# Optimization experiments

Measured on AMD Instinct MI355X. Metric: run time of the kernel, lower is better.

The kernel has to match this reference:

```python
import jax, jax.numpy as jnp
import numpy as np
import math

B, H, L, DK = 4, 12, 1024, 64
GLOBAL, LOCAL, INIT_VAL = 8, 4, 8
W = INIT_VAL + 1  # window length fed to each GRU
MAX_VAL = 1.0e12


def setup_inputs() -> dict:
    k0 = jax.random.key(0)
    ks = jax.random.split(k0, 9)
    bound = 1.0 / math.sqrt(DK)
    uni = lambda k, shape: jax.random.uniform(k, shape, jnp.float32, -bound, bound)
    return {
        "query": jax.random.normal(ks[0], (B, H, L, DK), jnp.float32),
        "key": jax.random.normal(ks[1], (B, H, L, DK), jnp.float32),
        "value": jax.random.normal(ks[2], (B, H, L, DK), jnp.float32),
        "mask": jax.random.randint(ks[3], (B, 1, L, L), 0, 2, jnp.int32),
        # per-local-head GRU parameters (torch nn.GRU layout: gates [r, z, n])
        "w_ih": uni(ks[4], (LOCAL, 3 * DK, DK)),
        "w_hh": uni(ks[5], (LOCAL, 3 * DK, DK)),
        "b_ih": uni(ks[6], (LOCAL, 3 * DK)),
        "b_hh": uni(ks[7], (LOCAL, 3 * DK)),
    }


def reference(query, key, value, mask, w_ih, w_hh, b_ih, b_hh):
    b, h, l, d_k = query.shape
    # ---- global softmax-attention heads ----
    q_g, k_g, v_g = query[:, :GLOBAL], key[:, :GLOBAL], value[:, :GLOBAL]
    scores = jnp.einsum('bhqd,bhkd->bhqk', q_g, k_g) / math.sqrt(d_k)
    scores = jnp.where(mask == 0, -MAX_VAL, scores)
    p_attn = jax.nn.softmax(scores, axis=-1)
    out_g = jnp.einsum('bhqk,bhkd->bhqd', p_attn, v_g)  # (b, GLOBAL, l, d_k)

    # ---- local heads: windowed value gather ----
    v_l = value[:, GLOBAL:]                                   # (b, LOCAL, l, d_k)
    v_pad = jnp.pad(v_l, ((0, 0), (0, 0), (0, INIT_VAL), (0, 0)))
    dist = jnp.arange(l)[:, None] + jnp.arange(W)[None, :]    # (l, W) forward window
    v_aug = v_pad[:, :, dist, :]                              # (b, LOCAL, l, W, d_k)
    x = v_aug.reshape(b * LOCAL * l, W, d_k)                  # all windows, shared by every GRU

    # ---- per-head GRU over the window; keep last hidden state ----
    def gru_last_hidden(wih, whh, bih, bhh):
        xg = jnp.einsum('ntd,gd->ntg', x, wih) + bih          # (N, W, 3*d_k), input gates precomputed
        def step(hc, xg_t):
            gh = hc @ whh.T + bhh
            xr, xz, xn = jnp.split(xg_t, 3, axis=-1)
            hr, hz, hn = jnp.split(gh, 3, axis=-1)
            r = jax.nn.sigmoid(xr + hr)
            z = jax.nn.sigmoid(xz + hz)
            n_ = jnp.tanh(xn + r * hn)
            return (1.0 - z) * n_ + z * hc, None
        h0 = jnp.zeros((x.shape[0], d_k), x.dtype)
        hT, _ = jax.lax.scan(step, h0, jnp.swapaxes(xg, 0, 1))
        return hT                                             # (N, d_k)

    hs = jax.vmap(gru_last_hidden)(w_ih, w_hh, b_ih, b_hh)    # (LOCAL, N, d_k)
    # faithful to torch cat: GRU i applied to ALL local heads -> LOCAL*LOCAL output heads
    out_l = hs.reshape(LOCAL, b, LOCAL, l, d_k).transpose(1, 0, 2, 3, 4)
    out_l = out_l.reshape(b, LOCAL * LOCAL, l, d_k)

    return jnp.concatenate([out_g, out_l], axis=1)            # (b, GLOBAL + LOCAL^2, l, d_k)
```

## Files before the change

### kernel.cpp

```cpp
#include <hip/hip_runtime.h>

#define B_  4
#define H_  12
#define L_  1024
#define DK_ 64
#define GH_ 8
#define WS_ 9

#define ATTN_LDS_BYTES (3 * 64 * 64 * 2)
#define GRU_W_OFF    0
#define GRU_XGP_OFF  24576
#define GRU_BIH_OFF  77888
#define GRU_BHH_OFF  78656
#define GRU_LDS_BYTES 79424
#define XGP_STRIDE   392

#define MB_WORDS (B_ * L_ * 16)

typedef __attribute__((ext_vector_type(8))) short short8;
typedef __attribute__((ext_vector_type(4))) float f32x4;

#define MFMA_BF16(a, b, c) __builtin_amdgcn_mfma_f32_16x16x32_bf16((a), (b), (c), 0, 0, 0)

__device__ __forceinline__ unsigned short f2bf(float f) {
  unsigned int u = __builtin_bit_cast(unsigned int, f);
  u += 0x7fffu + ((u >> 16) & 1u);
  return (unsigned short)(u >> 16);
}
__device__ __forceinline__ float bf2f(unsigned short s) {
  return __builtin_bit_cast(float, ((unsigned int)s) << 16);
}
__device__ __forceinline__ short8 pack8(const float4 a, const float4 b) {
  short8 r;
  r[0] = (short)f2bf(a.x); r[1] = (short)f2bf(a.y);
  r[2] = (short)f2bf(a.z); r[3] = (short)f2bf(a.w);
  r[4] = (short)f2bf(b.x); r[5] = (short)f2bf(b.y);
  r[6] = (short)f2bf(b.z); r[7] = (short)f2bf(b.w);
  return r;
}
__device__ __forceinline__ uint4 packrow16(const float4 a, const float4 b) {
  uint4 r;
  r.x = (unsigned)f2bf(a.x) | ((unsigned)f2bf(a.y) << 16);
  r.y = (unsigned)f2bf(a.z) | ((unsigned)f2bf(a.w) << 16);
  r.z = (unsigned)f2bf(b.x) | ((unsigned)f2bf(b.y) << 16);
  r.w = (unsigned)f2bf(b.z) | ((unsigned)f2bf(b.w) << 16);
  return r;
}
__device__ __forceinline__ float bfget(const uint2 u, const int r) {
  const unsigned d = (r & 2) ? u.y : u.x;
  return (r & 1) ? __builtin_bit_cast(float, d & 0xffff0000u)
                 : __builtin_bit_cast(float, d << 16);
}
__device__ __forceinline__ int pi_row(const int dt, const int m) {
  return ((dt & 1) << 5) + ((m >> 2) << 3) + ((dt >> 1) << 2) + (m & 3);
}

__global__ __launch_bounds__(256) void maskpack_kernel(
    const int* __restrict__ mask, unsigned long long* __restrict__ mb)
{
  const int idx = blockIdx.x * 256 + threadIdx.x;
  const int* src = mask + (size_t)idx * 64;
  unsigned long long bits = 0ull;
#pragma unroll
  for (int i = 0; i < 16; ++i) {
    const int4 m4 = *(const int4*)(src + i * 4);
    if (m4.x) bits |= 1ull << (i * 4 + 0);
    if (m4.y) bits |= 1ull << (i * 4 + 1);
    if (m4.z) bits |= 1ull << (i * 4 + 2);
    if (m4.w) bits |= 1ull << (i * 4 + 3);
  }
  mb[idx] = bits;
}

__global__ __launch_bounds__(256) void attn_kernel(
    const float* __restrict__ q, const float* __restrict__ k,
    const float* __restrict__ v, const int* __restrict__ mask,
    const unsigned long long* __restrict__ mb, const int use_bits,
    float* __restrict__ out)
{
  extern __shared__ char smc[];
  char* sK  = smc;
  char* sVT = smc + 8192;
  char* sP  = smc + 16384;

  const int tid = threadIdx.x;
  const int q0 = blockIdx.x * 64;
  const int h  = blockIdx.y;
  const int b  = blockIdx.z;

  const int w  = tid >> 6;
  const int ln = tid & 63;
  const int lg = ln >> 4;
  const int c  = ln & 15;

  const size_t hbase = ((size_t)b * H_ + h) * L_ * DK_;
  const float* kp = k + hbase;
  const float* vp = v + hbase;
  const int*   mp = mask + (size_t)b * L_ * L_;
  const unsigned long long* mbp = mb + (size_t)b * L_ * 16;

  short8 qa[2];
  {
    const float* qrow = q + hbase + (size_t)(q0 + w * 16 + c) * DK_ + lg * 8;
#pragma unroll
    for (int kt = 0; kt < 2; ++kt) {
      const float4 f0 = *(const float4*)(qrow + kt * 32);
      const float4 f1 = *(const float4*)(qrow + kt * 32 + 4);
      qa[kt] = pack8(f0, f1);
    }
  }

  char* sPw = sP + w * 2048;

  f32x4 o_[4];
#pragma unroll
  for (int nt = 0; nt < 4; ++nt) { o_[nt][0] = 0.f; o_[nt][1] = 0.f; o_[nt][2] = 0.f; o_[nt][3] = 0.f; }
  float mrun[4], lrun[4];
#pragma unroll
  for (int r = 0; r < 4; ++r) { mrun[r] = -1e30f; lrun[r] = 0.f; }

  const int rr  = tid >> 2;
  const int c16 = (tid & 3) << 4;
  const int r2  = (tid & 31) << 1;
  const int j0v = (tid >> 5) << 3;

  float4 kreg[4], vreg[4];
  unsigned long long mreg[4];
  {
    const float* ksrc = kp + (size_t)rr * DK_ + c16;
    kreg[0] = *(const float4*)(ksrc);      kreg[1] = *(const float4*)(ksrc + 4);
    kreg[2] = *(const float4*)(ksrc + 8);  kreg[3] = *(const float4*)(ksrc + 12);
    const float* vsrc = vp + (size_t)r2 * DK_ + j0v;
    vreg[0] = *(const float4*)(vsrc);       vreg[1] = *(const float4*)(vsrc + 4);
    vreg[2] = *(const float4*)(vsrc + 64);  vreg[3] = *(const float4*)(vsrc + 68);
    if (use_bits) {
#pragma unroll
      for (int r = 0; r < 4; ++r)
        mreg[r] = mbp[(size_t)(q0 + w * 16 + lg * 4 + r) * 16 + 0];
    }
  }

  for (int kt0 = 0; kt0 < 16; ++kt0) {
    {
      const int kb = rr * 128 + c16 * 2;
      const int sw = (rr & 7) << 4;
      *(uint4*)(sK + ((kb) ^ sw))      = packrow16(kreg[0], kreg[1]);
      *(uint4*)(sK + ((kb + 16) ^ sw)) = packrow16(kreg[2], kreg[3]);
      const float va_[8] = {vreg[0].x, vreg[0].y, vreg[0].z, vreg[0].w,
                            vreg[1].x, vreg[1].y, vreg[1].z, vreg[1].w};
      const float vb_[8] = {vreg[2].x, vreg[2].y, vreg[2].z, vreg[2].w,
                            vreg[3].x, vreg[3].y, vreg[3].z, vreg[3].w};
#pragma unroll
      for (int j = 0; j < 8; ++j) {
        const int d = j0v + j;
        const unsigned u32v = (unsigned)f2bf(va_[j]) | ((unsigned)f2bf(vb_[j]) << 16);
        *(unsigned*)(sVT + ((d * 128 + r2 * 2) ^ ((d & 7) << 4))) = u32v;
      }
    }
    asm volatile("s_waitcnt lgkmcnt(0)" ::: "memory");
    __builtin_amdgcn_s_barrier();

    unsigned long long mcur[4];
#pragma unroll
    for (int r = 0; r < 4; ++r) mcur[r] = mreg[r];
    {
      const int ktn = (kt0 + 1) & 15;
      const float* ksrc = kp + (size_t)(ktn * 64 + rr) * DK_ + c16;
      kreg[0] = *(const float4*)(ksrc);      kreg[1] = *(const float4*)(ksrc + 4);
      kreg[2] = *(const float4*)(ksrc + 8);  kreg[3] = *(const float4*)(ksrc + 12);
      const float* vsrc = vp + (size_t)(ktn * 64 + r2) * DK_ + j0v;
      vreg[0] = *(const float4*)(vsrc);       vreg[1] = *(const float4*)(vsrc + 4);
      vreg[2] = *(const float4*)(vsrc + 64);  vreg[3] = *(const float4*)(vsrc + 68);
      if (use_bits) {
#pragma unroll
        for (int r = 0; r < 4; ++r)
          mreg[r] = mbp[(size_t)(q0 + w * 16 + lg * 4 + r) * 16 + ktn];
      }
    }

    f32x4 acc[4];
#pragma unroll
    for (int nt = 0; nt < 4; ++nt) {
      acc[nt][0] = 0.f; acc[nt][1] = 0.f; acc[nt][2] = 0.f; acc[nt][3] = 0.f;
#pragma unroll
      for (int kt = 0; kt < 2; ++kt) {
        const int off = (((nt * 16 + c) * 128 + kt * 64 + lg * 16) ^ ((c & 7) << 4));
        const short8 bk = __builtin_bit_cast(short8, *(const uint4*)(sK + off));
        acc[nt] = MFMA_BF16(qa[kt], bk, acc[nt]);
      }
    }

#pragma unroll
    for (int r = 0; r < 4; ++r) {
      bool k0_, k1_, k2_, k3_;
      if (use_bits) {
        const unsigned long long mword = mcur[r];
        k0_ = (mword >> (c)) & 1ull;
        k1_ = (mword >> (16 + c)) & 1ull;
        k2_ = (mword >> (32 + c)) & 1ull;
        k3_ = (mword >> (48 + c)) & 1ull;
      } else {
        const int qr = q0 + w * 16 + lg * 4 + r;
        const int* mrow = mp + (size_t)qr * L_ + kt0 * 64 + c;
        k0_ = mrow[0] != 0; k1_ = mrow[16] != 0; k2_ = mrow[32] != 0; k3_ = mrow[48] != 0;
      }
      const float s0_ = k0_ ? acc[0][r] * 0.125f : -1e12f;
      const float s1_ = k1_ ? acc[1][r] * 0.125f : -1e12f;
      const float s2_ = k2_ ? acc[2][r] * 0.125f : -1e12f;
      const float s3_ = k3_ ? acc[3][r] * 0.125f : -1e12f;
      float mt = fmaxf(fmaxf(s0_, s1_), fmaxf(s2_, s3_));
#pragma unroll
      for (int off = 1; off < 16; off <<= 1) mt = fmaxf(mt, __shfl_xor(mt, off));
      const float mnew = fmaxf(mrun[r], mt);
      const float p0 = __expf(s0_ - mnew);
      const float p1 = __expf(s1_ - mnew);
      const float p2 = __expf(s2_ - mnew);
      const float p3 = __expf(s3_ - mnew);
      float pt = p0 + p1 + p2 + p3;
#pragma unroll
      for (int off = 1; off < 16; off <<= 1) pt += __shfl_xor(pt, off);
      const float scale = __expf(mrun[r] - mnew);
      mrun[r] = mnew;
      lrun[r] = lrun[r] * scale + pt;
      o_[0][r] *= scale; o_[1][r] *= scale; o_[2][r] *= scale; o_[3][r] *= scale;
      const int prow = lg * 4 + r;
      const int pb = prow * 128;
      const int psw = (prow & 7) << 4;
      *(unsigned short*)(sPw + ((pb + (c * 2)) ^ psw))       = f2bf(p0);
      *(unsigned short*)(sPw + ((pb + (16 + c) * 2) ^ psw))  = f2bf(p1);
      *(unsigned short*)(sPw + ((pb + (32 + c) * 2) ^ psw))  = f2bf(p2);
      *(unsigned short*)(sPw + ((pb + (48 + c) * 2) ^ psw))  = f2bf(p3);
    }

#pragma unroll
    for (int kt = 0; kt < 2; ++kt) {
      const int aoff = ((c * 128 + kt * 64 + lg * 16) ^ ((c & 7) << 4));
      const short8 pa = __builtin_bit_cast(short8, *(const uint4*)(sPw + aoff));
#pragma unroll
      for (int nt = 0; nt < 4; ++nt) {
        const int boff = (((nt * 16 + c) * 128 + kt * 64 + lg * 16) ^ ((c & 7) << 4));
        const short8 bv = __builtin_bit_cast(short8, *(const uint4*)(sVT + boff));
        o_[nt] = MFMA_BF16(pa, bv, o_[nt]);
      }
    }
    asm volatile("s_waitcnt lgkmcnt(0)" ::: "memory");
    __builtin_amdgcn_s_barrier();
  }

  float* op = out + (((size_t)b * 24 + h) * L_ + q0 + w * 16) * DK_;
#pragma unroll
  for (int r = 0; r < 4; ++r) {
    const float inv = 1.f / lrun[r];
#pragma unroll
    for (int nt = 0; nt < 4; ++nt)
      op[(size_t)(lg * 4 + r) * DK_ + nt * 16 + c] = o_[nt][r] * inv;
  }
}

__global__ __launch_bounds__(512, 4) void gru_kernel(
    const float* __restrict__ value, const float* __restrict__ wih_g,
    const float* __restrict__ whh_g, const float* __restrict__ bih_g,
    const float* __restrict__ bhh_g, float* __restrict__ out)
{
  extern __shared__ char smc[];
  char*  sW   = smc + GRU_W_OFF;
  char*  sXGP = smc + GRU_XGP_OFF;
  float* sBih = (float*)(smc + GRU_BIH_OFF);
  float* sBhh = (float*)(smc + GRU_BHH_OFF);

  const int tid  = threadIdx.x;
  const int l0   = blockIdx.x * 128;
  const int gset = blockIdx.y >> 2;
  const int vh   = blockIdx.y & 3;
  const int b    = blockIdx.z;

  const float* vp   = value + (((size_t)b * H_ + GH_ + vh) * L_) * DK_;
  const float* wih  = wih_g + (size_t)gset * 192 * DK_;
  const float* whh  = whh_g + (size_t)gset * 192 * DK_;
  const float* bihp = bih_g + gset * 192;
  const float* bhhp = bhh_g + gset * 192;

  if (tid < 192) { sBih[tid] = bihp[tid]; sBhh[tid] = bhhp[tid]; }

  for (int cid = tid; cid < 1536; cid += 512) {
    const int row = cid >> 3, ch = cid & 7;
    const int g = row >> 6, dt = (row >> 4) & 3, m = row & 15;
    const int arow = g * 64 + pi_row(dt, m);
    const float* wp = whh + (size_t)arow * 64 + ch * 8;
    const float4 w0 = *(const float4*)wp;
    const float4 w1 = *(const float4*)(wp + 4);
    *(uint4*)(sW + ((row * 128 + ch * 16) ^ ((row & 7) << 4))) = packrow16(w0, w1);
  }
  __syncthreads();

  const int w  = tid >> 6;
  const int ln = tid & 63;
  const int lg = ln >> 4;
  const int c  = ln & 15;

  for (int t = w; t < 108; t += 8) {
    const int jt = t % 12, pt = t / 12;
    const int g = jt >> 2, dt = jt & 3;
    const int aj = g * 64 + pi_row(dt, c);
    const float* wb = wih + (size_t)aj * 64 + lg * 8;
    const short8 aA = pack8(*(const float4*)(wb),      *(const float4*)(wb + 4));
    const short8 aB = pack8(*(const float4*)(wb + 32), *(const float4*)(wb + 36));
    const int pos = pt * 16 + c;
    const int gp  = l0 + pos;
    const bool valid = gp < L_;
    float4 z4; z4.x = 0.f; z4.y = 0.f; z4.z = 0.f; z4.w = 0.f;
    const float* va = vp + (size_t)gp * 64 + lg * 8;
    const short8 bA = pack8(valid ? *(const float4*)(va)      : z4,
                            valid ? *(const float4*)(va + 4)  : z4);
    const short8 bB = pack8(valid ? *(const float4*)(va + 32) : z4,
                            valid ? *(const float4*)(va + 36) : z4);
    f32x4 acc = {0.f, 0.f, 0.f, 0.f};
    acc = MFMA_BF16(aA, bA, acc);
    acc = MFMA_BF16(aB, bB, acc);
    const int jb = g * 64 + ((dt & 1) << 5) + (lg << 3) + ((dt >> 1) << 2);
    const f32x4 bi = *(const f32x4*)(sBih + jb);
    const f32x4 bh4 = *(const f32x4*)(sBhh + jb);
    const float foldh = (g < 2) ? 1.f : 0.f;
    if (pos < 136) {
      uint2 pk;
      pk.x = (unsigned)f2bf(acc[0] + bi[0] + foldh * bh4[0]) |
             ((unsigned)f2bf(acc[1] + bi[1] + foldh * bh4[1]) << 16);
      pk.y = (unsigned)f2bf(acc[2] + bi[2] + foldh * bh4[2]) |
             ((unsigned)f2bf(acc[3] + bi[3] + foldh * bh4[3]) << 16);
      *(uint2*)(sXGP + pos * XGP_STRIDE + jt * 32 + lg * 8) = pk;
    }
  }
  __syncthreads();

  const int seqB = w * 16;
  const int xrow0 = seqB + c;

  f32x4 bhn[4];
#pragma unroll
  for (int dt = 0; dt < 4; ++dt)
    bhn[dt] = *(const f32x4*)(sBhh + 128 + ((dt & 1) << 5) + (lg << 3) + ((dt >> 1) << 2));

  float hfr[4][4];
  short8 bh[2], bl[2];
#pragma unroll
  for (int dt = 0; dt < 4; ++dt)
#pragma unroll
    for (int r = 0; r < 4; ++r) hfr[dt][r] = 0.f;
#pragma unroll
  for (int kt = 0; kt < 2; ++kt) {
#pragma unroll
    for (int i = 0; i < 8; ++i) { bh[kt][i] = 0; bl[kt][i] = 0; }
  }

  const int swz = (c & 7) << 4;

  for (int ts = 0; ts < WS_; ++ts) {
    const int xbase = (xrow0 + ts) * XGP_STRIDE + lg * 8;

#pragma unroll
    for (int dt = 0; dt < 4; ++dt) {
      const uint2 xgr = *(const uint2*)(sXGP + xbase + dt * 32);
      const uint2 xgz = *(const uint2*)(sXGP + xbase + (4 + dt) * 32);
      const uint2 xgn = *(const uint2*)(sXGP + xbase + (8 + dt) * 32);

      f32x4 ar = {0.f, 0.f, 0.f, 0.f};
      f32x4 az = {0.f, 0.f, 0.f, 0.f};
      f32x4 an = {0.f, 0.f, 0.f, 0.f};
#pragma unroll
      for (int kt = 0; kt < 2; ++kt) {
        const int base = kt * 64 + lg * 16;
        const short8 wr = __builtin_bit_cast(short8,
            *(const uint4*)(sW + ((((dt)     * 16 + c) * 128 + base) ^ swz)));
        const short8 wz = __builtin_bit_cast(short8,
            *(const uint4*)(sW + ((((4 + dt) * 16 + c) * 128 + base) ^ swz)));
        const short8 wn = __builtin_bit_cast(short8,
            *(const uint4*)(sW + ((((8 + dt) * 16 + c) * 128 + base) ^ swz)));
        ar = MFMA_BF16(wr, bh[kt], ar); ar = MFMA_BF16(wr, bl[kt], ar);
        az = MFMA_BF16(wz, bh[kt], az); az = MFMA_BF16(wz, bl[kt], az);
        an = MFMA_BF16(wn, bh[kt], an); an = MFMA_BF16(wn, bl[kt], an);
      }

#pragma unroll
      for (int r = 0; r < 4; ++r) {
        const float xr = bfget(xgr, r);
        const float xz = bfget(xgz, r);
        const float xn = bfget(xgn, r);
        const float rr_ = __builtin_amdgcn_rcpf(1.f + __expf(-(xr + ar[r])));
        const float zz  = __builtin_amdgcn_rcpf(1.f + __expf(-(xz + az[r])));
        const float hn  = an[r] + bhn[dt][r];
        const float e2  = __expf(2.f * (xn + rr_ * hn));
        const float nn  = 1.f - 2.f * __builtin_amdgcn_rcpf(1.f + e2);
        hfr[dt][r] = (1.f - zz) * nn + zz * hfr[dt][r];
      }
    }

#pragma unroll
    for (int kt = 0; kt < 2; ++kt) {
      short8 hi8, lo8;
#pragma unroll
      for (int i = 0; i < 8; ++i) {
        const float hv = (i < 4) ? hfr[kt][i] : hfr[kt + 2][i - 4];
        const unsigned short hb16 = f2bf(hv);
        hi8[i] = (short)hb16;
        lo8[i] = (short)f2bf(hv - bf2f(hb16));
      }
      bh[kt] = hi8; bl[kt] = lo8;
    }
  }

  float* op = out + (((size_t)b * 24 + (GH_ + gset * 4 + vh)) * L_ + l0 + seqB + c) * DK_;
#pragma unroll
  for (int dt = 0; dt < 4; ++dt)
#pragma unroll
    for (int r = 0; r < 4; ++r) {
      const int dact = ((dt & 1) << 5) + (lg << 3) + ((dt >> 1) << 2) + r;
      op[dact] = hfr[dt][r];
    }
}

extern "C" void kernel_launch(void* const* d_in, const int* in_sizes, int n_in,
                              void* d_out, int out_size, void* d_ws, size_t ws_size,
                              hipStream_t stream) {
  (void)in_sizes; (void)n_in; (void)out_size;
  const float* q   = (const float*)d_in[0];
  const float* k   = (const float*)d_in[1];
  const float* v   = (const float*)d_in[2];
  const int*   msk = (const int*)d_in[3];
  const float* wih = (const float*)d_in[4];
  const float* whh = (const float*)d_in[5];
  const float* bih = (const float*)d_in[6];
  const float* bhh = (const float*)d_in[7];
  float* out = (float*)d_out;

  const int use_bits = (ws_size >= (size_t)MB_WORDS * 8) ? 1 : 0;
  unsigned long long* mb = (unsigned long long*)d_ws;

  (void)hipFuncSetAttribute((const void*)gru_kernel,
                            hipFuncAttributeMaxDynamicSharedMemorySize, GRU_LDS_BYTES);

  if (use_bits)
    maskpack_kernel<<<dim3(MB_WORDS / 256), dim3(256), 0, stream>>>(msk, mb);
  attn_kernel<<<dim3(L_ / 64, GH_, B_), dim3(256), ATTN_LDS_BYTES, stream>>>(
      q, k, v, msk, mb, use_bits, out);
  gru_kernel<<<dim3(L_ / 128, 16, B_), dim3(512), GRU_LDS_BYTES, stream>>>(
      v, wih, whh, bih, bhh, out);
}
```

Baseline: 346.5 us.

## Halve GRU block tile and hoist recurrent weights into registers

```diff
diff --git a/kernel.cpp b/kernel.cpp
--- a/kernel.cpp
+++ b/kernel.cpp
@@ -10,9 +10,9 @@
 #define ATTN_LDS_BYTES (3 * 64 * 64 * 2)
 #define GRU_W_OFF    0
 #define GRU_XGP_OFF  24576
-#define GRU_BIH_OFF  77888
-#define GRU_BHH_OFF  78656
-#define GRU_LDS_BYTES 79424
+#define GRU_BIH_OFF  52800
+#define GRU_BHH_OFF  53568
+#define GRU_LDS_BYTES 54336
 #define XGP_STRIDE   392
 
 #define MB_WORDS (B_ * L_ * 16)
@@ -257,7 +257,7 @@
   }
 }
 
-__global__ __launch_bounds__(512, 4) void gru_kernel(
+__global__ __launch_bounds__(256, 2) void gru_kernel(
     const float* __restrict__ value, const float* __restrict__ wih_g,
     const float* __restrict__ whh_g, const float* __restrict__ bih_g,
     const float* __restrict__ bhh_g, float* __restrict__ out)
@@ -269,7 +269,7 @@
   float* sBhh = (float*)(smc + GRU_BHH_OFF);
 
   const int tid  = threadIdx.x;
-  const int l0   = blockIdx.x * 128;
+  const int l0   = blockIdx.x * 64;
   const int gset = blockIdx.y >> 2;
   const int vh   = blockIdx.y & 3;
   const int b    = blockIdx.z;
@@ -282,7 +282,7 @@
 
   if (tid < 192) { sBih[tid] = bihp[tid]; sBhh[tid] = bhhp[tid]; }
 
-  for (int cid = tid; cid < 1536; cid += 512) {
+  for (int cid = tid; cid < 1536; cid += 256) {
     const int row = cid >> 3, ch = cid & 7;
     const int g = row >> 6, dt = (row >> 4) & 3, m = row & 15;
     const int arow = g * 64 + pi_row(dt, m);
@@ -298,7 +298,7 @@
   const int lg = ln >> 4;
   const int c  = ln & 15;
 
-  for (int t = w; t < 108; t += 8) {
+  for (int t = w; t < 60; t += 4) {
     const int jt = t % 12, pt = t / 12;
     const int g = jt >> 2, dt = jt & 3;
     const int aj = g * 64 + pi_row(dt, c);
@@ -321,7 +321,7 @@
     const f32x4 bi = *(const f32x4*)(sBih + jb);
     const f32x4 bh4 = *(const f32x4*)(sBhh + jb);
     const float foldh = (g < 2) ? 1.f : 0.f;
-    if (pos < 136) {
+    if (pos < 72) {
       uint2 pk;
       pk.x = (unsigned)f2bf(acc[0] + bi[0] + foldh * bh4[0]) |
              ((unsigned)f2bf(acc[1] + bi[1] + foldh * bh4[1]) << 16);
@@ -332,6 +332,15 @@
   }
   __syncthreads();
 
+  const int swz = (c & 7) << 4;
+  short8 wreg[12][2];
+#pragma unroll
+  for (int jt = 0; jt < 12; ++jt)
+#pragma unroll
+    for (int kt = 0; kt < 2; ++kt)
+      wreg[jt][kt] = __builtin_bit_cast(short8,
+          *(const uint4*)(sW + ((((jt * 16 + c) * 128) + kt * 64 + lg * 16) ^ swz)));
+
   const int seqB = w * 16;
   const int xrow0 = seqB + c;
 
@@ -352,39 +361,32 @@
     for (int i = 0; i < 8; ++i) { bh[kt][i] = 0; bl[kt][i] = 0; }
   }
 
-  const int swz = (c & 7) << 4;
-
   for (int ts = 0; ts < WS_; ++ts) {
     const int xbase = (xrow0 + ts) * XGP_STRIDE + lg * 8;
+    uint2 xg[12];
+#pragma unroll
+    for (int jt = 0; jt < 12; ++jt)
+      xg[jt] = *(const uint2*)(sXGP + xbase + jt * 32);
 
 #pragma unroll
     for (int dt = 0; dt < 4; ++dt) {
-      const uint2 xgr = *(const uint2*)(sXGP + xbase + dt * 32);
-      const uint2 xgz = *(const uint2*)(sXGP + xbase + (4 + dt) * 32);
-      const uint2 xgn = *(const uint2*)(sXGP + xbase + (8 + dt) * 32);
-
       f32x4 ar = {0.f, 0.f, 0.f, 0.f};
       f32x4 az = {0.f, 0.f, 0.f, 0.f};
       f32x4 an = {0.f, 0.f, 0.f, 0.f};
 #pragma unroll
       for (int kt = 0; kt < 2; ++kt) {
-        const int base = kt * 64 + lg * 16;
-        const short8 wr = __builtin_bit_cast(short8,
-            *(const uint4*)(sW + ((((dt)     * 16 + c) * 128 + base) ^ swz)));
-        const short8 wz = __builtin_bit_cast(short8,
-            *(const uint4*)(sW + ((((4 + dt) * 16 + c) * 128 + base) ^ swz)));
-        const short8 wn = __builtin_bit_cast(short8,
-            *(const uint4*)(sW + ((((8 + dt) * 16 + c) * 128 + base) ^ swz)));
-        ar = MFMA_BF16(wr, bh[kt], ar); ar = MFMA_BF16(wr, bl[kt], ar);
-        az = MFMA_BF16(wz, bh[kt], az); az = MFMA_BF16(wz, bl[kt], az);
-        an = MFMA_BF16(wn, bh[kt], an); an = MFMA_BF16(wn, bl[kt], an);
-      }
-
+        ar = MFMA_BF16(wreg[dt][kt],     bh[kt], ar);
+        ar = MFMA_BF16(wreg[dt][kt],     bl[kt], ar);
+        az = MFMA_BF16(wreg[4 + dt][kt], bh[kt], az);
+        az = MFMA_BF16(wreg[4 + dt][kt], bl[kt], az);
+        an = MFMA_BF16(wreg[8 + dt][kt], bh[kt], an);
+        an = MFMA_BF16(wreg[8 + dt][kt], bl[kt], an);
+      }
 #pragma unroll
       for (int r = 0; r < 4; ++r) {
-        const float xr = bfget(xgr, r);
-        const float xz = bfget(xgz, r);
-        const float xn = bfget(xgn, r);
+        const float xr = bfget(xg[dt], r);
+        const float xz = bfget(xg[4 + dt], r);
+        const float xn = bfget(xg[8 + dt], r);
         const float rr_ = __builtin_amdgcn_rcpf(1.f + __expf(-(xr + ar[r])));
         const float zz  = __builtin_amdgcn_rcpf(1.f + __expf(-(xz + az[r])));
         const float hn  = an[r] + bhn[dt][r];
@@ -442,6 +444,6 @@
     maskpack_kernel<<<dim3(MB_WORDS / 256), dim3(256), 0, stream>>>(msk, mb);
   attn_kernel<<<dim3(L_ / 64, GH_, B_), dim3(256), ATTN_LDS_BYTES, stream>>>(
       q, k, v, msk, mb, use_bits, out);
-  gru_kernel<<<dim3(L_ / 128, 16, B_), dim3(512), GRU_LDS_BYTES, stream>>>(
+  gru_kernel<<<dim3(L_ / 64, 16, B_), dim3(256), GRU_LDS_BYTES, stream>>>(
       v, wih, whh, bih, bhh, out);
 }
```

Measured after the change: 309.9 us. 1.12x faster.
